# Optimization experiments

Measured on AMD Instinct MI355X. Metric: run time of the kernel, lower is better.

## Reference

```python
import jax, jax.numpy as jnp
import numpy as np

N_NODES = 100000
EPS = 1e-5  # BatchNorm1d default eps


def gcn_conv(x, W, b, row, col, n):
    """PyG GCNConv: add self-loops, symmetric normalization, linear, scatter-add."""
    loop = jnp.arange(n, dtype=row.dtype)
    row_f = jnp.concatenate([row, loop])  # sources
    col_f = jnp.concatenate([col, loop])  # targets
    # degree of target nodes (edge_weight = 1)
    deg = jax.ops.segment_sum(jnp.ones_like(col_f, dtype=x.dtype), col_f, num_segments=n)
    dinv = jnp.where(deg > 0, jax.lax.rsqrt(deg), 0.0)
    norm = dinv[row_f] * dinv[col_f]  # [E+N]
    h = x @ W  # [N, out]
    msg = h[row_f] * norm[:, None]  # [E+N, out]
    out = jax.ops.segment_sum(msg, col_f, num_segments=n)
    return out + b


def batch_norm(x, gamma, beta):
    # training-mode BatchNorm1d: biased batch stats over node axis
    mean = jnp.mean(x, axis=0)
    var = jnp.var(x, axis=0)
    return (x - mean) * jax.lax.rsqrt(var + EPS) * gamma + beta


def setup_inputs() -> dict:
    key = jax.random.key(0)
    ks = jax.random.split(key, 8)
    n, e, f_in, h = N_NODES, 1600000, 25, 128
    x = jax.random.normal(ks[0], (n, f_in), dtype=jnp.float32)
    edge_index = jax.random.randint(ks[1], (2, e), 0, n, dtype=jnp.int64)
    s1 = 1.0 / np.sqrt(f_in)
    s2 = 1.0 / np.sqrt(h)
    W1 = jax.random.uniform(ks[2], (f_in, h), jnp.float32, -s1, s1)
    b1 = jax.random.uniform(ks[3], (h,), jnp.float32, -s1, s1)
    gamma = jnp.ones((h,), jnp.float32)
    beta = jnp.zeros((h,), jnp.float32)
    W2 = jax.random.uniform(ks[4], (h, h), jnp.float32, -s2, s2)
    b2 = jax.random.uniform(ks[5], (h,), jnp.float32, -s2, s2)
    return {"x": x, "edge_index": edge_index, "W1": W1, "b1": b1,
            "gamma": gamma, "beta": beta, "W2": W2, "b2": b2}


def reference(x, edge_index, W1, b1, gamma, beta, W2, b2):
    row, col = edge_index[0], edge_index[1]
    n = x.shape[0]
    h = jax.nn.relu(gcn_conv(x, W1, b1, row, col, n))
    h = batch_norm(h, gamma, beta)
    h = jax.nn.relu(gcn_conv(h, W2, b2, row, col, n))
    return h
```

## Files before the change

### kernel.cpp

```cpp
#include <hip/hip_runtime.h>
#include <stdint.h>


#define HID 128
#define NBB 512

typedef short bf16x8 __attribute__((ext_vector_type(8)));
typedef float f32x4 __attribute__((ext_vector_type(4)));

__device__ __forceinline__ unsigned short f2bf(float f) {
    unsigned int u = __float_as_uint(f);
    unsigned int r = (u + 0x7FFFu + ((u >> 16) & 1u)) >> 16;
    return (unsigned short)r;
}
__device__ __forceinline__ unsigned int pack2bf(float lo, float hi) {
    return (unsigned int)f2bf(lo) | ((unsigned int)f2bf(hi) << 16);
}
__device__ __forceinline__ float bflo(unsigned int v) { return __uint_as_float(v << 16); }
__device__ __forceinline__ float bfhi(unsigned int v) { return __uint_as_float(v & 0xffff0000u); }

__global__ void detect_kernel(const unsigned int* __restrict__ w, int* __restrict__ mode, int nwords) {
    __shared__ int any;
    if (threadIdx.x == 0) any = 0;
    __syncthreads();
    for (int i = threadIdx.x * 2 + 1; i < nwords && i < 8192; i += 512) {
        if (w[i] != 0) atomicOr(&any, 1);
    }
    __syncthreads();
    if (threadIdx.x == 0) *mode = any ? 0 : 1;
}

__device__ __forceinline__ int load_idx(const void* ei, size_t i, int mode) {
    return mode ? (int)((const long long*)ei)[i] : ((const int*)ei)[i];
}

__global__ __launch_bounds__(256) void count_q_kernel(const void* __restrict__ ei,
                                                      const int* __restrict__ modep,
                                                      int* __restrict__ qcnt,
                                                      int E, int CHUNK, int nchunk) {
    __shared__ int qc[512];
    for (int i = threadIdx.x; i < nchunk; i += 256) qc[i] = 0;
    __syncthreads();
    int mode = *modep;
    int beg = blockIdx.x * CHUNK;
    int end = beg + CHUNK; if (end > E) end = E;
    for (int e = beg + threadIdx.x; e < end; e += 256) {
        int c = load_idx(ei, (size_t)E + e, mode);
        atomicAdd(&qc[c >> 8], 1);
    }
    __syncthreads();
    for (int i = threadIdx.x; i < nchunk; i += 256)
        qcnt[blockIdx.x * nchunk + i] = qc[i];
}

__global__ __launch_bounds__(256) void scanq_partial_kernel(const int* __restrict__ qcnt,
                                                            int* __restrict__ blocksum,
                                                            int NQ, int nchunk) {
    int j0 = blockIdx.x * 2048 + threadIdx.x * 8;
    int s = 0;
    #pragma unroll
    for (int i = 0; i < 8; ++i) {
        int j = j0 + i;
        if (j < NQ) {
            int q = j >> 9, b = j & (NBB - 1);
            s += qcnt[b * nchunk + q];
        }
    }
    #pragma unroll
    for (int off = 32; off > 0; off >>= 1) s += __shfl_down(s, off);
    __shared__ int ls[4];
    if ((threadIdx.x & 63) == 0) ls[threadIdx.x >> 6] = s;
    __syncthreads();
    if (threadIdx.x == 0) blocksum[blockIdx.x] = ls[0] + ls[1] + ls[2] + ls[3];
}

__global__ __launch_bounds__(1024) void scanq_blocksums_kernel(const int* __restrict__ blocksum,
                                                               int* __restrict__ blockoff,
                                                               int* __restrict__ qoff,
                                                               int nsb, int NQ) {
    __shared__ int s[1024];
    int t = threadIdx.x;
    int own = (t < nsb) ? blocksum[t] : 0;
    s[t] = own;
    __syncthreads();
    for (int off = 1; off < 1024; off <<= 1) {
        int v = s[t] + ((t >= off) ? s[t - off] : 0);
        __syncthreads();
        s[t] = v;
        __syncthreads();
    }
    if (t < nsb) blockoff[t] = s[t] - own;
    if (t == 1023) qoff[NQ] = s[1023];
}

__global__ __launch_bounds__(256) void scanq_finalize_kernel(const int* __restrict__ qcnt,
                                                             const int* __restrict__ blockoff,
                                                             int* __restrict__ qoff,
                                                             int NQ, int nchunk) {
    int t = threadIdx.x;
    int j0 = blockIdx.x * 2048 + t * 8;
    int v[8], own = 0;
    #pragma unroll
    for (int i = 0; i < 8; ++i) {
        int j = j0 + i;
        v[i] = 0;
        if (j < NQ) {
            int q = j >> 9, b = j & (NBB - 1);
            v[i] = qcnt[b * nchunk + q];
        }
        own += v[i];
    }
    __shared__ int s[256];
    s[t] = own;
    __syncthreads();
    for (int off = 1; off < 256; off <<= 1) {
        int x = s[t] + ((t >= off) ? s[t - off] : 0);
        __syncthreads();
        s[t] = x;
        __syncthreads();
    }
    int e = blockoff[blockIdx.x] + s[t] - own;
    #pragma unroll
    for (int i = 0; i < 8; ++i) {
        int j = j0 + i;
        if (j < NQ) qoff[j] = e;
        e += v[i];
    }
}

__global__ __launch_bounds__(256) void bin_kernel(const void* __restrict__ ei,
                                                  const int* __restrict__ modep,
                                                  const int* __restrict__ qoff,
                                                  unsigned int* __restrict__ packed,
                                                  int E, int CHUNK, int nchunk) {
    __shared__ int cur[512];
    for (int i = threadIdx.x; i < nchunk; i += 256)
        cur[i] = qoff[i * NBB + blockIdx.x];
    __syncthreads();
    int mode = *modep;
    int beg = blockIdx.x * CHUNK;
    int end = beg + CHUNK; if (end > E) end = E;
    for (int e = beg + threadIdx.x; e < end; e += 256) {
        int c = load_idx(ei, (size_t)E + e, mode);
        int r = load_idx(ei, (size_t)e, mode);
        int pos = atomicAdd(&cur[c >> 8], 1);
        packed[pos] = ((unsigned)(c & 255) << 24) | (unsigned)r;
    }
}

__global__ __launch_bounds__(256) void chunk_build_kernel(
    const unsigned int* __restrict__ packed, const int* __restrict__ qoff,
    int* __restrict__ rowptr, float* __restrict__ dinv,
    int* __restrict__ edge_src, int n, int E) {
    int q = blockIdx.x;
    int t = threadIdx.x;
    int pbeg = qoff[q * NBB];
    int pend = qoff[(q + 1) * NBB];
    __shared__ int cnt256[256], cur[256], s[256];
    cnt256[t] = 0;
    __syncthreads();
    for (int i = pbeg + t; i < pend; i += 256)
        atomicAdd(&cnt256[packed[i] >> 24], 1);
    __syncthreads();
    int own = cnt256[t];
    s[t] = own;
    __syncthreads();
    for (int off = 1; off < 256; off <<= 1) {
        int x = s[t] + ((t >= off) ? s[t - off] : 0);
        __syncthreads();
        s[t] = x;
        __syncthreads();
    }
    int pref = s[t] - own;
    int node = (q << 8) + t;
    if (node < n) {
        rowptr[node] = pbeg + pref;
        dinv[node] = rsqrtf((float)(own + 1));
    }
    cur[t] = pbeg + pref;
    if (q == gridDim.x - 1 && t == 0) rowptr[n] = E;
    __syncthreads();
    for (int i = pbeg + t; i < pend; i += 256) {
        unsigned int u = packed[i];
        int pos = atomicAdd(&cur[u >> 24], 1);
        edge_src[pos] = (int)(u & 0xFFFFFFu);
    }
}

__global__ __launch_bounds__(256) void xpad_kernel(const float* __restrict__ x,
                                                   unsigned int* __restrict__ xp, int n) {
    int r = blockIdx.x * 256 + threadIdx.x;
    if (r >= n) return;
    const float* xr = x + (size_t)r * 25;
    unsigned int* o = xp + (size_t)r * 16;
    #pragma unroll
    for (int j = 0; j < 12; ++j)
        o[j] = pack2bf(xr[j * 2], xr[j * 2 + 1]);
    o[12] = pack2bf(xr[24], 0.f);
    o[13] = 0u; o[14] = 0u; o[15] = 0u;
}

__global__ __launch_bounds__(256) void prop_x_kernel(
    const unsigned int* __restrict__ xp, const int* __restrict__ rowptr,
    const int* __restrict__ edge_src, const float* __restrict__ dinv,
    unsigned int* __restrict__ y0, int n) {
    int wid = (blockIdx.x * 256 + threadIdx.x) >> 6;
    if (wid >= n) return;
    int lane = threadIdx.x & 63;
    int g = lane >> 4, i = lane & 15;
    int beg = rowptr[wid], end = rowptr[wid + 1];
    float dc = dinv[wid];
    float ax = 0.f, ay = 0.f;
    for (int b = beg; b < end; b += 64) {
        int m = end - b; if (m > 64) m = 64;
        int s = 0; float w = 0.f;
        if (lane < m) { s = edge_src[b + lane]; w = dinv[s]; }
        int nsteps = (m + 3) >> 2;
        for (int t = 0; t < nsteps; ++t) {
            int e = 4 * t + g;
            int sj = __shfl(s, e & 63);
            float wj = __shfl(w, e & 63);
            if (e >= m) { sj = 0; wj = 0.f; }
            unsigned int u = xp[(size_t)sj * 16 + i];
            ax = fmaf(bflo(u), wj, ax);
            ay = fmaf(bfhi(u), wj, ay);
        }
    }
    if (g == 0) {
        unsigned int u = xp[(size_t)wid * 16 + i];
        ax = fmaf(bflo(u), dc, ax);
        ay = fmaf(bfhi(u), dc, ay);
    }
    ax += __shfl_xor(ax, 16); ax += __shfl_xor(ax, 32);
    ay += __shfl_xor(ay, 16); ay += __shfl_xor(ay, 32);
    if (lane < 16)
        y0[(size_t)wid * 16 + i] = pack2bf(ax * dc, ay * dc);
}

__global__ __launch_bounds__(256) void gemm1_kernel(const unsigned int* __restrict__ y0,
                                                    const float* __restrict__ W,
                                                    const float* __restrict__ bias,
                                                    unsigned short* __restrict__ y1,
                                                    float* __restrict__ bnsum,
                                                    float* __restrict__ bnsumsq, int n) {
    __shared__ float lw[25 * HID];
    for (int i = threadIdx.x; i < 25 * HID; i += 256) lw[i] = W[i];
    __syncthreads();
    int g = threadIdx.x >> 7, c = threadIdx.x & 127;
    float bc = bias[c];
    float s = 0.f, s2 = 0.f;
    for (int r = blockIdx.x * 2 + g; r < n; r += gridDim.x * 2) {
        const unsigned int* yr = y0 + (size_t)r * 16;
        float acc = bc;
        #pragma unroll
        for (int j = 0; j < 12; ++j) {
            unsigned int u = yr[j];
            acc = fmaf(bflo(u), lw[(j * 2 + 0) * HID + c], acc);
            acc = fmaf(bfhi(u), lw[(j * 2 + 1) * HID + c], acc);
        }
        acc = fmaf(bflo(yr[12]), lw[24 * HID + c], acc);
        acc = fmaxf(acc, 0.f);
        y1[(size_t)r * HID + c] = f2bf(acc);
        s += acc;
        s2 = fmaf(acc, acc, s2);
    }
    __shared__ float ls[256], ls2[256];
    ls[threadIdx.x] = s; ls2[threadIdx.x] = s2;
    __syncthreads();
    if (threadIdx.x < 128) {
        atomicAdd(&bnsum[c], ls[threadIdx.x] + ls[threadIdx.x + 128]);
        atomicAdd(&bnsumsq[c], ls2[threadIdx.x] + ls2[threadIdx.x + 128]);
    }
}

__global__ __launch_bounds__(256) void propagate_kernel(
    const unsigned short* __restrict__ h, const int* __restrict__ rowptr,
    const int* __restrict__ edge_src, const float* __restrict__ dinv,
    const float* __restrict__ bias, float* __restrict__ out, int n) {
    int wid = (blockIdx.x * 256 + threadIdx.x) >> 6;
    if (wid >= n) return;
    int lane = threadIdx.x & 63;
    int beg = rowptr[wid], end = rowptr[wid + 1];
    float dc = dinv[wid];
    float ax = 0.f, ay = 0.f;
    const unsigned int* hp = (const unsigned int*)h;
    for (int b = beg; b < end; b += 64) {
        int m = end - b; if (m > 64) m = 64;
        int s = 0; float w = 0.f;
        if (lane < m) { s = edge_src[b + lane]; w = dinv[s]; }
        int j = 0;
        for (; j + 8 <= m; j += 8) {
            int s0 = __shfl(s, j + 0), s1 = __shfl(s, j + 1);
            int s2 = __shfl(s, j + 2), s3 = __shfl(s, j + 3);
            int s4 = __shfl(s, j + 4), s5 = __shfl(s, j + 5);
            int s6 = __shfl(s, j + 6), s7 = __shfl(s, j + 7);
            unsigned int v0 = hp[(size_t)s0 * 64 + lane];
            unsigned int v1 = hp[(size_t)s1 * 64 + lane];
            unsigned int v2 = hp[(size_t)s2 * 64 + lane];
            unsigned int v3 = hp[(size_t)s3 * 64 + lane];
            unsigned int v4 = hp[(size_t)s4 * 64 + lane];
            unsigned int v5 = hp[(size_t)s5 * 64 + lane];
            unsigned int v6 = hp[(size_t)s6 * 64 + lane];
            unsigned int v7 = hp[(size_t)s7 * 64 + lane];
            float w0 = __shfl(w, j + 0), w1 = __shfl(w, j + 1);
            float w2 = __shfl(w, j + 2), w3 = __shfl(w, j + 3);
            float w4 = __shfl(w, j + 4), w5 = __shfl(w, j + 5);
            float w6 = __shfl(w, j + 6), w7 = __shfl(w, j + 7);
            ax = fmaf(bflo(v0), w0, ax); ay = fmaf(bfhi(v0), w0, ay);
            ax = fmaf(bflo(v1), w1, ax); ay = fmaf(bfhi(v1), w1, ay);
            ax = fmaf(bflo(v2), w2, ax); ay = fmaf(bfhi(v2), w2, ay);
            ax = fmaf(bflo(v3), w3, ax); ay = fmaf(bfhi(v3), w3, ay);
            ax = fmaf(bflo(v4), w4, ax); ay = fmaf(bfhi(v4), w4, ay);
            ax = fmaf(bflo(v5), w5, ax); ay = fmaf(bfhi(v5), w5, ay);
            ax = fmaf(bflo(v6), w6, ax); ay = fmaf(bfhi(v6), w6, ay);
            ax = fmaf(bflo(v7), w7, ax); ay = fmaf(bfhi(v7), w7, ay);
        }
        for (; j < m; ++j) {
            int sj = __shfl(s, j);
            float wj = __shfl(w, j);
            unsigned int v = hp[(size_t)sj * 64 + lane];
            ax = fmaf(bflo(v), wj, ax);
            ay = fmaf(bfhi(v), wj, ay);
        }
    }
    {
        unsigned int v = hp[(size_t)wid * 64 + lane];
        ax = fmaf(bflo(v), dc, ax);
        ay = fmaf(bfhi(v), dc, ay);
    }
    float bx = bias[lane * 2], by = bias[lane * 2 + 1];
    ax = fmaxf(fmaf(ax, dc, bx), 0.f);
    ay = fmaxf(fmaf(ay, dc, by), 0.f);
    *(float2*)(out + (size_t)wid * HID + lane * 2) = make_float2(ax, ay);
}

__global__ void bn_finalize_kernel(const float* __restrict__ sum, const float* __restrict__ sumsq,
                                   const float* __restrict__ gamma, const float* __restrict__ beta,
                                   float* __restrict__ scale, float* __restrict__ shift, float inv_n) {
    int c = threadIdx.x;
    float mean = sum[c] * inv_n;
    float var = sumsq[c] * inv_n - mean * mean;
    float sc = gamma[c] * rsqrtf(var + 1e-5f);
    scale[c] = sc;
    shift[c] = beta[c] - mean * sc;
}

__global__ __launch_bounds__(256) void wt_kernel(const float* __restrict__ W,
                                                 unsigned short* __restrict__ Wt) {
    int idx = blockIdx.x * 256 + threadIdx.x;
    int c = idx >> 7, k = idx & 127;
    Wt[c * 128 + k] = f2bf(W[k * 128 + c]);
}

__global__ __launch_bounds__(256) void gemm2_mfma_kernel(
    const unsigned short* __restrict__ yb, const unsigned short* __restrict__ Wt,
    const float* __restrict__ scale, const float* __restrict__ shift,
    unsigned short* __restrict__ out, int n) {
    __shared__ unsigned short lwt[128 * 136];
    __shared__ unsigned short ly[128 * 136];
    int t = threadIdx.x;
    int base = blockIdx.x * 128;

    {
        const unsigned int* w32 = (const unsigned int*)Wt;
        unsigned int* l32 = (unsigned int*)lwt;
        #pragma unroll
        for (int i = 0; i < 32; ++i) {
            int idx = t + i * 256;
            int r = idx >> 6, cp = idx & 63;
            l32[r * 68 + cp] = w32[r * 64 + cp];
        }
    }
    {
        int r = t >> 1, hh = t & 1;
        int gr = base + r;
        unsigned int* l32 = (unsigned int*)ly;
        const uint4* yrow = (const uint4*)(yb + (size_t)gr * HID + hh * 64);
        #pragma unroll
        for (int j = 0; j < 8; ++j) {
            uint4 u = make_uint4(0u, 0u, 0u, 0u);
            if (gr < n) u = yrow[j];
            int gk = hh * 64 + j * 8;
            float a0 = fmaf(bflo(u.x), scale[gk + 0], shift[gk + 0]);
            float a1 = fmaf(bfhi(u.x), scale[gk + 1], shift[gk + 1]);
            float a2 = fmaf(bflo(u.y), scale[gk + 2], shift[gk + 2]);
            float a3 = fmaf(bfhi(u.y), scale[gk + 3], shift[gk + 3]);
            float a4 = fmaf(bflo(u.z), scale[gk + 4], shift[gk + 4]);
            float a5 = fmaf(bfhi(u.z), scale[gk + 5], shift[gk + 5]);
            float a6 = fmaf(bflo(u.w), scale[gk + 6], shift[gk + 6]);
            float a7 = fmaf(bfhi(u.w), scale[gk + 7], shift[gk + 7]);
            l32[r * 68 + hh * 32 + j * 4 + 0] = pack2bf(a0, a1);
            l32[r * 68 + hh * 32 + j * 4 + 1] = pack2bf(a2, a3);
            l32[r * 68 + hh * 32 + j * 4 + 2] = pack2bf(a4, a5);
            l32[r * 68 + hh * 32 + j * 4 + 3] = pack2bf(a6, a7);
        }
    }
    __syncthreads();

    int w = t >> 6, lane = t & 63;
    int li = lane & 15, lg = lane >> 4;
    f32x4 acc[2][8];
    #pragma unroll
    for (int a = 0; a < 2; ++a)
        #pragma unroll
        for (int b = 0; b < 8; ++b) acc[a][b] = (f32x4){0.f, 0.f, 0.f, 0.f};

    #pragma unroll
    for (int ks = 0; ks < 4; ++ks) {
        int kb = ks * 32 + lg * 8;
        bf16x8 af[2], bfr[8];
        #pragma unroll
        for (int rt = 0; rt < 2; ++rt)
            af[rt] = *(const bf16x8*)&ly[(w * 32 + rt * 16 + li) * 136 + kb];
        #pragma unroll
        for (int cf = 0; cf < 8; ++cf)
            bfr[cf] = *(const bf16x8*)&lwt[(cf * 16 + li) * 136 + kb];
        #pragma unroll
        for (int rt = 0; rt < 2; ++rt)
            #pragma unroll
            for (int cf = 0; cf < 8; ++cf)
                acc[rt][cf] = __builtin_amdgcn_mfma_f32_16x16x32_bf16(
                    af[rt], bfr[cf], acc[rt][cf], 0, 0, 0);
    }

    #pragma unroll
    for (int rt = 0; rt < 2; ++rt) {
        #pragma unroll
        for (int reg = 0; reg < 4; ++reg) {
            int gr = base + w * 32 + rt * 16 + lg * 4 + reg;
            if (gr < n) {
                #pragma unroll
                for (int cf = 0; cf < 8; ++cf)
                    out[(size_t)gr * HID + cf * 16 + li] = f2bf(acc[rt][cf][reg]);
            }
        }
    }
}

extern "C" void kernel_launch(void* const* d_in, const int* in_sizes, int n_in,
                              void* d_out, int out_size, void* d_ws, size_t ws_size,
                              hipStream_t stream) {
    const float* x     = (const float*)d_in[0];
    const void*  ei    = d_in[1];
    const float* W1    = (const float*)d_in[2];
    const float* b1    = (const float*)d_in[3];
    const float* gamma = (const float*)d_in[4];
    const float* beta  = (const float*)d_in[5];
    const float* W2    = (const float*)d_in[6];
    const float* b2    = (const float*)d_in[7];
    float* out = (float*)d_out;

    const int f_in = 25;
    int n = in_sizes[0] / f_in;
    int E = in_sizes[1] / 2;
    int nchunk = (n + 255) >> 8;
    int NQ = nchunk * NBB;
    int nsb = (NQ + 2047) / 2048;
    int CHUNK = (E + NBB - 1) / NBB;

    char* ws = (char*)d_ws;
    size_t off = 0;
    auto alloc = [&](size_t bytes) -> void* {
        void* p = ws + off;
        off += (bytes + 511) & ~(size_t)511;
        return p;
    };
    int*   rowptr    = (int*)alloc(((size_t)n + 1) * 4);
    float* dinv      = (float*)alloc((size_t)n * 4);
    int*   edge_src  = (int*)alloc((size_t)E * 4);
    unsigned int* packed = (unsigned int*)alloc((size_t)E * 4);
    int*   qcnt      = (int*)alloc((size_t)NQ * 4);
    int*   qoff      = (int*)alloc(((size_t)NQ + 1) * 4);
    int*   blocksum  = (int*)alloc((size_t)nsb * 4);
    int*   blockoff  = (int*)alloc((size_t)nsb * 4);
    float* bnacc     = (float*)alloc(256 * 4);
    float* sclshift  = (float*)alloc(256 * 4);
    int*   mode      = (int*)alloc(4);
    unsigned int* xp   = (unsigned int*)alloc((size_t)n * 16 * 4);
    unsigned int* y0   = (unsigned int*)alloc((size_t)n * 16 * 4);
    unsigned short* y1 = (unsigned short*)alloc((size_t)n * HID * 2);
    unsigned short* Wt = (unsigned short*)alloc(128 * 128 * 2);
    unsigned short* h  = (unsigned short*)alloc((size_t)n * HID * 2);

    hipMemsetAsync(bnacc, 0, 256 * 4, stream);

    detect_kernel<<<1, 256, 0, stream>>>((const unsigned int*)ei, mode, 2 * E);
    count_q_kernel<<<NBB, 256, 0, stream>>>(ei, mode, qcnt, E, CHUNK, nchunk);
    scanq_partial_kernel<<<nsb, 256, 0, stream>>>(qcnt, blocksum, NQ, nchunk);
    scanq_blocksums_kernel<<<1, 1024, 0, stream>>>(blocksum, blockoff, qoff, nsb, NQ);
    scanq_finalize_kernel<<<nsb, 256, 0, stream>>>(qcnt, blockoff, qoff, NQ, nchunk);
    bin_kernel<<<NBB, 256, 0, stream>>>(ei, mode, qoff, packed, E, CHUNK, nchunk);
    chunk_build_kernel<<<nchunk, 256, 0, stream>>>(packed, qoff, rowptr, dinv, edge_src, n, E);

    xpad_kernel<<<(n + 255) / 256, 256, 0, stream>>>(x, xp, n);
    prop_x_kernel<<<(n + 3) / 4, 256, 0, stream>>>(xp, rowptr, edge_src, dinv, y0, n);
    gemm1_kernel<<<1024, 256, 0, stream>>>(y0, W1, b1, y1, bnacc, bnacc + 128, n);

    bn_finalize_kernel<<<1, 128, 0, stream>>>(bnacc, bnacc + 128, gamma, beta,
                                              sclshift, sclshift + 128, 1.0f / (float)n);

    wt_kernel<<<64, 256, 0, stream>>>(W2, Wt);
    gemm2_mfma_kernel<<<(n + 127) / 128, 256, 0, stream>>>(y1, Wt, sclshift, sclshift + 128, h, n);
    propagate_kernel<<<(n + 3) / 4, 256, 0, stream>>>(h, rowptr, edge_src, dinv, b2, out, n);
}
```

Before: 264.9 us.

## Fuse layer-1 feature propagation with the dense transform and batch-norm statistics

Merges the layer-1 neighbour aggregation over padded bf16 inputs with the 25x128 linear, ReLU and batch-norm sum/sum-of-squares into one grid-stride kernel. The aggregated 25-wide row stays in registers and is broadcast by shuffles, so the y0 intermediate buffer and one kernel launch go away. The final propagation kernel also drops its scalar tail loop and always runs the 8-way unrolled body. Out-of-range lanes carry source 0 with zero weight, so the result is unchanged, at the cost of some redundant loads of node 0. The fused kernel has fewer waves (1024 blocks in a grid-stride loop) and holds more shared memory per block.

New measurement: 255.5 us. -3.6%, faster.

```diff
diff --git a/kernel.cpp b/kernel.cpp
--- a/kernel.cpp
+++ b/kernel.cpp
@@ -200,76 +200,75 @@
     o[13] = 0u; o[14] = 0u; o[15] = 0u;
 }
 
-__global__ __launch_bounds__(256) void prop_x_kernel(
+__global__ __launch_bounds__(256) void l1_kernel(
     const unsigned int* __restrict__ xp, const int* __restrict__ rowptr,
     const int* __restrict__ edge_src, const float* __restrict__ dinv,
-    unsigned int* __restrict__ y0, int n) {
-    int wid = (blockIdx.x * 256 + threadIdx.x) >> 6;
-    if (wid >= n) return;
+    const float* __restrict__ W, const float* __restrict__ bias,
+    unsigned short* __restrict__ y1, float* __restrict__ bnsum,
+    float* __restrict__ bnsumsq, int n) {
+    __shared__ float lw[25 * HID];
+    __shared__ float lb[HID];
+    for (int i = threadIdx.x; i < 25 * HID; i += 256) lw[i] = W[i];
+    if (threadIdx.x < HID) lb[threadIdx.x] = bias[threadIdx.x];
+    __syncthreads();
     int lane = threadIdx.x & 63;
     int g = lane >> 4, i = lane & 15;
-    int beg = rowptr[wid], end = rowptr[wid + 1];
-    float dc = dinv[wid];
-    float ax = 0.f, ay = 0.f;
-    for (int b = beg; b < end; b += 64) {
-        int m = end - b; if (m > 64) m = 64;
-        int s = 0; float w = 0.f;
-        if (lane < m) { s = edge_src[b + lane]; w = dinv[s]; }
-        int nsteps = (m + 3) >> 2;
-        for (int t = 0; t < nsteps; ++t) {
-            int e = 4 * t + g;
-            int sj = __shfl(s, e & 63);
-            float wj = __shfl(w, e & 63);
-            if (e >= m) { sj = 0; wj = 0.f; }
-            unsigned int u = xp[(size_t)sj * 16 + i];
-            ax = fmaf(bflo(u), wj, ax);
-            ay = fmaf(bfhi(u), wj, ay);
-        }
-    }
-    if (g == 0) {
-        unsigned int u = xp[(size_t)wid * 16 + i];
-        ax = fmaf(bflo(u), dc, ax);
-        ay = fmaf(bfhi(u), dc, ay);
-    }
-    ax += __shfl_xor(ax, 16); ax += __shfl_xor(ax, 32);
-    ay += __shfl_xor(ay, 16); ay += __shfl_xor(ay, 32);
-    if (lane < 16)
-        y0[(size_t)wid * 16 + i] = pack2bf(ax * dc, ay * dc);
-}
-
-__global__ __launch_bounds__(256) void gemm1_kernel(const unsigned int* __restrict__ y0,
-                                                    const float* __restrict__ W,
-                                                    const float* __restrict__ bias,
-                                                    unsigned short* __restrict__ y1,
-                                                    float* __restrict__ bnsum,
-                                                    float* __restrict__ bnsumsq, int n) {
-    __shared__ float lw[25 * HID];
-    for (int i = threadIdx.x; i < 25 * HID; i += 256) lw[i] = W[i];
-    __syncthreads();
-    int g = threadIdx.x >> 7, c = threadIdx.x & 127;
-    float bc = bias[c];
-    float s = 0.f, s2 = 0.f;
-    for (int r = blockIdx.x * 2 + g; r < n; r += gridDim.x * 2) {
-        const unsigned int* yr = y0 + (size_t)r * 16;
-        float acc = bc;
-        #pragma unroll
-        for (int j = 0; j < 12; ++j) {
-            unsigned int u = yr[j];
-            acc = fmaf(bflo(u), lw[(j * 2 + 0) * HID + c], acc);
-            acc = fmaf(bfhi(u), lw[(j * 2 + 1) * HID + c], acc);
-        }
-        acc = fmaf(bflo(yr[12]), lw[24 * HID + c], acc);
-        acc = fmaxf(acc, 0.f);
-        y1[(size_t)r * HID + c] = f2bf(acc);
-        s += acc;
-        s2 = fmaf(acc, acc, s2);
-    }
-    __shared__ float ls[256], ls2[256];
-    ls[threadIdx.x] = s; ls2[threadIdx.x] = s2;
-    __syncthreads();
-    if (threadIdx.x < 128) {
-        atomicAdd(&bnsum[c], ls[threadIdx.x] + ls[threadIdx.x + 128]);
-        atomicAdd(&bnsumsq[c], ls2[threadIdx.x] + ls2[threadIdx.x + 128]);
+    int wid0 = (blockIdx.x * 256 + threadIdx.x) >> 6;
+    float s0 = 0.f, q0 = 0.f, s1 = 0.f, q1 = 0.f;
+    for (int node = wid0; node < n; node += 4096) {
+        int beg = rowptr[node], end = rowptr[node + 1];
+        float dc = dinv[node];
+        float ax = 0.f, ay = 0.f;
+        for (int b = beg; b < end; b += 64) {
+            int m = end - b; if (m > 64) m = 64;
+            int s = 0; float w = 0.f;
+            if (lane < m) { s = edge_src[b + lane]; w = dinv[s]; }
+            int nsteps = (m + 3) >> 2;
+            for (int t = 0; t < nsteps; ++t) {
+                int e = 4 * t + g;
+                int sj = __shfl(s, e);
+                float wj = __shfl(w, e);
+                unsigned int u = xp[(size_t)sj * 16 + i];
+                ax = fmaf(bflo(u), wj, ax);
+                ay = fmaf(bfhi(u), wj, ay);
+            }
+        }
+        if (g == 0) {
+            unsigned int u = xp[(size_t)node * 16 + i];
+            ax = fmaf(bflo(u), dc, ax);
+            ay = fmaf(bfhi(u), dc, ay);
+        }
+        ax += __shfl_xor(ax, 16); ax += __shfl_xor(ax, 32);
+        ay += __shfl_xor(ay, 16); ay += __shfl_xor(ay, 32);
+        ax *= dc; ay *= dc;
+        float acc0 = lb[lane], acc1 = lb[lane + 64];
+        #pragma unroll
+        for (int k = 0; k < 25; ++k) {
+            float yk = (k & 1) ? __shfl(ay, k >> 1) : __shfl(ax, k >> 1);
+            acc0 = fmaf(yk, lw[k * HID + lane], acc0);
+            acc1 = fmaf(yk, lw[k * HID + lane + 64], acc1);
+        }
+        acc0 = fmaxf(acc0, 0.f);
+        acc1 = fmaxf(acc1, 0.f);
+        y1[(size_t)node * HID + lane] = f2bf(acc0);
+        y1[(size_t)node * HID + lane + 64] = f2bf(acc1);
+        s0 += acc0; q0 = fmaf(acc0, acc0, q0);
+        s1 += acc1; q1 = fmaf(acc1, acc1, q1);
+    }
+    __shared__ float r0[256], r1[256], r2[256], r3[256];
+    r0[threadIdx.x] = s0; r1[threadIdx.x] = q0;
+    r2[threadIdx.x] = s1; r3[threadIdx.x] = q1;
+    __syncthreads();
+    if (threadIdx.x < 64) {
+        int l = threadIdx.x;
+        float a = r0[l] + r0[l + 64] + r0[l + 128] + r0[l + 192];
+        float b = r1[l] + r1[l + 64] + r1[l + 128] + r1[l + 192];
+        float c = r2[l] + r2[l + 64] + r2[l + 128] + r2[l + 192];
+        float d = r3[l] + r3[l + 64] + r3[l + 128] + r3[l + 192];
+        atomicAdd(&bnsum[l], a);
+        atomicAdd(&bnsumsq[l], b);
+        atomicAdd(&bnsum[l + 64], c);
+        atomicAdd(&bnsumsq[l + 64], d);
     }
 }
 
@@ -288,8 +287,7 @@
         int m = end - b; if (m > 64) m = 64;
         int s = 0; float w = 0.f;
         if (lane < m) { s = edge_src[b + lane]; w = dinv[s]; }
-        int j = 0;
-        for (; j + 8 <= m; j += 8) {
+        for (int j = 0; j < m; j += 8) {
             int s0 = __shfl(s, j + 0), s1 = __shfl(s, j + 1);
             int s2 = __shfl(s, j + 2), s3 = __shfl(s, j + 3);
             int s4 = __shfl(s, j + 4), s5 = __shfl(s, j + 5);
@@ -315,13 +313,6 @@
             ax = fmaf(bflo(v6), w6, ax); ay = fmaf(bfhi(v6), w6, ay);
             ax = fmaf(bflo(v7), w7, ax); ay = fmaf(bfhi(v7), w7, ay);
         }
-        for (; j < m; ++j) {
-            int sj = __shfl(s, j);
-            float wj = __shfl(w, j);
-            unsigned int v = hp[(size_t)sj * 64 + lane];
-            ax = fmaf(bflo(v), wj, ax);
-            ay = fmaf(bfhi(v), wj, ay);
-        }
     }
     {
         unsigned int v = hp[(size_t)wid * 64 + lane];
@@ -477,7 +468,6 @@
     float* sclshift  = (float*)alloc(256 * 4);
     int*   mode      = (int*)alloc(4);
     unsigned int* xp   = (unsigned int*)alloc((size_t)n * 16 * 4);
-    unsigned int* y0   = (unsigned int*)alloc((size_t)n * 16 * 4);
     unsigned short* y1 = (unsigned short*)alloc((size_t)n * HID * 2);
     unsigned short* Wt = (unsigned short*)alloc(128 * 128 * 2);
     unsigned short* h  = (unsigned short*)alloc((size_t)n * HID * 2);
@@ -493,8 +483,8 @@
     chunk_build_kernel<<<nchunk, 256, 0, stream>>>(packed, qoff, rowptr, dinv, edge_src, n, E);
 
     xpad_kernel<<<(n + 255) / 256, 256, 0, stream>>>(x, xp, n);
-    prop_x_kernel<<<(n + 3) / 4, 256, 0, stream>>>(xp, rowptr, edge_src, dinv, y0, n);
-    gemm1_kernel<<<1024, 256, 0, stream>>>(y0, W1, b1, y1, bnacc, bnacc + 128, n);
+    l1_kernel<<<1024, 256, 0, stream>>>(xp, rowptr, edge_src, dinv, W1, b1,
+                                        y1, bnacc, bnacc + 128, n);
 
     bn_finalize_kernel<<<1, 128, 0, stream>>>(bnacc, bnacc + 128, gamma, beta,
                                               sclshift, sclshift + 128, 1.0f / (float)n);
```
